# Kernel tuning notes

Hardware: AMD Instinct MI355X
Metric: run time of the kernel (lower is better)

## Reference

```python
import jax, jax.numpy as jnp
import numpy as np

N, E = 20000, 160000
F, H, OUT = 256, 8, 128
L = 6            # total layers -> 5 GAT layers
LM1 = L - 1
NGN = L // 3 + 1 # 3 GraphNorms
D = F // H       # 32 per head
GN_FREQ = 3
EPS = 1e-5


def setup_inputs() -> dict:
    key = jax.random.key(0)
    ks = jax.random.split(key, 12)
    x = jax.random.normal(ks[0], (N, 1), dtype=jnp.float32)
    edge_index = jax.random.randint(ks[1], (2, E), 0, N, dtype=jnp.int32)
    W0 = jax.random.normal(ks[2], (1, F), dtype=jnp.float32) * 0.1
    b0 = jnp.zeros((F,), jnp.float32)
    gat_lin = jax.random.normal(ks[3], (LM1, F, F), dtype=jnp.float32) * (1.0 / np.sqrt(F))
    att_src = jax.random.normal(ks[4], (LM1, H, D), dtype=jnp.float32) * 0.1
    att_dst = jax.random.normal(ks[5], (LM1, H, D), dtype=jnp.float32) * 0.1
    gat_bias = jnp.zeros((LM1, F), jnp.float32)
    gn_weight = jnp.ones((NGN, F), jnp.float32)
    gn_bias = jnp.zeros((NGN, F), jnp.float32)
    gn_mean_scale = jnp.ones((NGN, F), jnp.float32)
    lin_W = jax.random.normal(ks[6], (F, OUT), dtype=jnp.float32) * (1.0 / np.sqrt(F))
    lin_b = jnp.zeros((OUT,), jnp.float32)
    return {"x": x, "W0": W0, "b0": b0, "gat_lin": gat_lin, "att_src": att_src,
            "att_dst": att_dst, "gat_bias": gat_bias, "gn_weight": gn_weight,
            "gn_bias": gn_bias, "gn_mean_scale": gn_mean_scale,
            "lin_W": lin_W, "lin_b": lin_b, "edge_index": edge_index}


def _gcn_conv(x, W, b, src, dst, n):
    h = x @ W
    deg = jax.ops.segment_sum(jnp.ones(src.shape[0], h.dtype), dst, num_segments=n)
    dinv = jnp.where(deg > 0, jax.lax.rsqrt(deg), 0.0)
    norm = dinv[src] * dinv[dst]                      # [E']
    out = jax.ops.segment_sum(h[src] * norm[:, None], dst, num_segments=n)
    return out + b


def _gat_conv(x, W, a_src, a_dst, src, dst, n):
    # PyG GATConv (concat=True, negative_slope=0.2, self-loops in src/dst)
    h = (x @ W).reshape(n, H, D)
    s = jnp.einsum('nhd,hd->nh', h, a_src)            # [N,H]
    t = jnp.einsum('nhd,hd->nh', h, a_dst)
    e = jax.nn.leaky_relu(s[src] + t[dst], 0.2)       # [E',H]
    m = jax.ops.segment_max(e, dst, num_segments=n)   # per-dst softmax
    e = jnp.exp(e - m[dst])
    denom = jax.ops.segment_sum(e, dst, num_segments=n)
    alpha = e / (denom[dst] + 1e-16)
    out = jax.ops.segment_sum(h[src] * alpha[:, :, None], dst, num_segments=n)
    return out.reshape(n, F)


def _graph_norm(x, w, b, ms):
    # PyG GraphNorm with batch=None (single graph): per-feature stats over nodes
    mean = jnp.mean(x, axis=0)
    out = x - ms * mean
    var = jnp.mean(out * out, axis=0)
    return w * out * jax.lax.rsqrt(var + EPS) + b


def reference(x, W0, b0, gat_lin, att_src, att_dst, gat_bias, gn_weight, gn_bias,
              gn_mean_scale, lin_W, lin_b, edge_index):
    n = x.shape[0]
    loops = jnp.arange(n, dtype=edge_index.dtype)
    src = jnp.concatenate([edge_index[0], loops])
    dst = jnp.concatenate([edge_index[1], loops])
    h = jax.nn.relu(_gcn_conv(x, W0, b0, src, dst, n))
    for i in range(LM1):
        if i % GN_FREQ == 0:
            g = i // GN_FREQ
            h = _graph_norm(h, gn_weight[g], gn_bias[g], gn_mean_scale[g])
        out = _gat_conv(h, gat_lin[i], att_src[i], att_dst[i], src, dst, n)
        if i % GN_FREQ == 0:
            out = out + gat_bias[i]
        h = h + jax.nn.relu(out)
    return h @ lin_W + lin_b
```

## Files before the change

kernel.cpp:

```cpp
#include <hip/hip_runtime.h>
#include <hip/hip_bf16.h>
#include <stdint.h>

typedef float f32x4 __attribute__((ext_vector_type(4)));
typedef short s16x8 __attribute__((ext_vector_type(8)));

__device__ __forceinline__ float bf2f(unsigned short u) {
    union { unsigned int i; float f; } v; v.i = ((unsigned int)u) << 16; return v.f;
}
__device__ __forceinline__ unsigned short f2bf(float f) {
    union { float f; unsigned int i; } v; v.f = f;
    unsigned int x = v.i;
    return (unsigned short)((x + 0x7fffu + ((x >> 16) & 1u)) >> 16);
}
__device__ __forceinline__ void bfp(unsigned int u, float& lo, float& hi) {
    union { unsigned int i; float f; } a, b;
    a.i = u << 16; b.i = u & 0xffff0000u;
    lo = a.f; hi = b.f;
}
__device__ __forceinline__ void gload16(const void* g, void* l) {
    __builtin_amdgcn_global_load_lds(
        (const __attribute__((address_space(1))) void*)g,
        (__attribute__((address_space(3))) void*)l, 16, 0, 0);
}

__global__ void k_prep(const int* __restrict__ ei, int E, int* __restrict__ deg,
                       int CB,
                       const float* __restrict__ gat_lin,
                       const float* __restrict__ lin_W,
                       const float* __restrict__ att_src,
                       const float* __restrict__ att_dst,
                       unsigned short* __restrict__ Wt,
                       unsigned short* __restrict__ lt) {
    int bid = blockIdx.x;
    if (bid < CB) {
        int e = bid * 256 + threadIdx.x;
        if (e < E) atomicAdd(&deg[ei[E + e]], 1);
        return;
    }
    int idx = (bid - CB) * 256 + threadIdx.x;
    const int T1 = 5 * 65536;
    const int T2 = T1 + 128 * 256;
    const int T3 = T2 + 5 * 64 * 256;
    if (idx < T1) {
        int l = idx >> 16, r = idx & 0xFFFF;
        int k = r >> 8, nrow = r & 255;
        Wt[(size_t)l * 81920 + nrow * 256 + k] =
            f2bf(gat_lin[(size_t)l * 65536 + k * 256 + nrow]);
    } else if (idx < T2) {
        int j = idx - T1;
        int k = j >> 7, nrow = j & 127;
        lt[nrow * 256 + k] = f2bf(lin_W[(size_t)k * 128 + nrow]);
    } else if (idx < T3) {
        int j = idx - T2;
        int l = j >> 14, r = j & 16383;
        int row = r >> 8, k = r & 255;
        float v = 0.f;
        if (row < 16) {
            int head = row & 7;
            const float* a = (row < 8) ? (att_src + l * 256 + head * 32)
                                       : (att_dst + l * 256 + head * 32);
            const float* wr = gat_lin + (size_t)l * 65536 + k * 256 + head * 32;
#pragma unroll
            for (int d = 0; d < 32; ++d) v += wr[d] * a[d];
        }
        Wt[(size_t)l * 81920 + (256 + row) * 256 + k] = f2bf(v);
    }
}

__global__ __launch_bounds__(256) void k_emit(const int* __restrict__ deg,
                                              int* __restrict__ rowptr,
                                              int* __restrict__ wo,
                                              float* __restrict__ dinv, int n) {
    __shared__ int buf[256];
    int t = threadIdx.x;
    int bid = blockIdx.x;
    int lim = bid * 256;
    int s = 0;
    for (int i = t; i < lim; i += 256) s += deg[i] + 1;
    buf[t] = s;
    __syncthreads();
#pragma unroll
    for (int off = 128; off > 0; off >>= 1) {
        if (t < off) buf[t] += buf[t + off];
        __syncthreads();
    }
    int boff = buf[0];
    __syncthreads();
    int i = bid * 256 + t;
    int v = (i < n) ? deg[i] + 1 : 0;
    buf[t] = v;
    __syncthreads();
    for (int off = 1; off < 256; off <<= 1) {
        int add = (t >= off) ? buf[t - off] : 0;
        __syncthreads();
        buf[t] += add;
        __syncthreads();
    }
    if (i < n) {
        int excl = boff + buf[t] - v;
        rowptr[i] = excl;
        wo[i] = excl;
        dinv[i] = rsqrtf((float)v);
        if (i == n - 1) rowptr[n] = excl + v;
    }
}

__global__ void k_fill(const int* __restrict__ ei, int E, int n,
                       int* wo, int* srcs) {
    int e = blockIdx.x * blockDim.x + threadIdx.x;
    int EP = E + n;
    if (e >= EP) return;
    int s_, d_;
    if (e < E) { s_ = ei[e]; d_ = ei[E + e]; }
    else       { s_ = d_ = e - E; }
    int pos = atomicAdd(&wo[d_], 1);
    srcs[pos] = s_;
}

__global__ __launch_bounds__(256) void k_h0f(const float* __restrict__ x,
                                             const float* __restrict__ dinv,
                                             const int* __restrict__ rowptr,
                                             const int* __restrict__ srcs,
                                             const float* __restrict__ W0,
                                             const float* __restrict__ b0,
                                             unsigned short* __restrict__ hbf,
                                             int n, int Mpad) {
    int wave = threadIdx.x >> 6, lane = threadIdx.x & 63;
    int node = blockIdx.x * 4 + wave;
    if (node >= Mpad) return;
    size_t base = (size_t)node * 256 + lane * 4;
    if (node >= n) {
        ushort4 z = {0, 0, 0, 0};
        *reinterpret_cast<ushort4*>(hbf + base) = z;
        return;
    }
    int p0 = rowptr[node], p1 = rowptr[node + 1];
    float sum = 0.f;
    for (int p = p0 + lane; p < p1; p += 64) {
        int s = srcs[p];
        sum += x[s] * dinv[s];
    }
#pragma unroll
    for (int m = 1; m < 64; m <<= 1) sum += __shfl_xor(sum, m);
    float sv = sum * dinv[node];
    float4 wv = *reinterpret_cast<const float4*>(W0 + lane * 4);
    float4 bv = *reinterpret_cast<const float4*>(b0 + lane * 4);
    ushort4 o;
    o.x = f2bf(fmaxf(sv * wv.x + bv.x, 0.f));
    o.y = f2bf(fmaxf(sv * wv.y + bv.y, 0.f));
    o.z = f2bf(fmaxf(sv * wv.z + bv.z, 0.f));
    o.w = f2bf(fmaxf(sv * wv.w + bv.w, 0.f));
    *reinterpret_cast<ushort4*>(hbf + base) = o;
}

__global__ __launch_bounds__(256) void k_gn_reduce(const unsigned short* __restrict__ hbf,
                                                   float* sums, float* sumsq, int n) {
    int f = threadIdx.x;
    float s = 0.f, q = 0.f;
    for (int r = blockIdx.x; r < n; r += gridDim.x) {
        float v = bf2f(hbf[(size_t)r * 256 + f]);
        s += v; q += v * v;
    }
    atomicAdd(&sums[f], s);
    atomicAdd(&sumsq[f], q);
}

__global__ __launch_bounds__(256) void k_gnfold(const float* __restrict__ st,
                                                const float* __restrict__ w,
                                                const float* __restrict__ b,
                                                const float* __restrict__ ms,
                                                unsigned short* __restrict__ Wt,
                                                float* __restrict__ so,
                                                float* __restrict__ rowbias,
                                                float ninv) {
    __shared__ float red[256];
    int col = blockIdx.x, k = threadIdx.x;
    float mean = st[k] * ninv;
    float m2   = st[256 + k] * ninv;
    float msf  = ms[k];
    float var  = m2 + msf * mean * mean * (msf - 2.0f);
    float sc = w[k] * rsqrtf(var + 1e-5f);
    float of = b[k] - msf * mean * sc;
    size_t idx = (size_t)col * 256 + k;
    float wv = bf2f(Wt[idx]);
    red[k] = of * wv;
    __syncthreads();
#pragma unroll
    for (int off = 128; off > 0; off >>= 1) {
        if (k < off) red[k] += red[k + off];
        __syncthreads();
    }
    if (k == 0) rowbias[col] = red[0];
    Wt[idx] = f2bf(sc * wv);
    if (col == 0) { so[k] = sc; so[256 + k] = of; }
}

#define BM 64
__global__ __launch_bounds__(512) void k_gemm_mfma(
    const unsigned short* __restrict__ A,
    const unsigned short* __restrict__ Bt,
    unsigned short* __restrict__ Cb,
    float* __restrict__ Cf,
    float* __restrict__ sbuf,
    float* __restrict__ tbuf,
    const float* __restrict__ bias,
    const float* __restrict__ rowbias,
    int M, int ldc)
{
    __shared__ unsigned short As[64 * 256];
    __shared__ unsigned short Bs[64 * 256];
    const int tid = threadIdx.x;
    const int bm = blockIdx.x * BM;
    const int bn = blockIdx.y * 64;
    {
        const char* ga = (const char*)(A + (size_t)bm * 256);
        const char* gb = (const char*)(Bt + (size_t)bn * 256);
        char* la = (char*)As;
        char* lb = (char*)Bs;
#pragma unroll
        for (int i = 0; i < 4; ++i) {
            int o  = (i * 512 + tid) * 16;
            int so = o ^ (((o >> 9) & 7) << 4);
            gload16(ga + so, la + o);
            gload16(gb + so, lb + o);
        }
    }
    __syncthreads();

    const int lane = tid & 63;
    const int w  = tid >> 6;
    const int wm = (w >> 1) * 16;
    const int wn = (w & 1) * 32;
    const int r  = lane & 15, kb = lane >> 4;
    const int r4 = (lane >> 4) * 4, cc = lane & 15;
    const char* la = (const char*)As;
    const char* lb = (const char*)Bs;

    f32x4 acc[2] = {};
#pragma unroll
    for (int ks = 0; ks < 8; ++ks) {
        int row = wm + r;
        int c16 = (ks * 4 + kb) ^ (row & 7);
        s16x8 af = *(const s16x8*)(la + row * 512 + c16 * 16);
#pragma unroll
        for (int j = 0; j < 2; ++j) {
            int col = wn + j * 16 + r;
            int d16 = (ks * 4 + kb) ^ (col & 7);
            s16x8 bfr = *(const s16x8*)(lb + col * 512 + d16 * 16);
            acc[j] = __builtin_amdgcn_mfma_f32_16x16x32_bf16(af, bfr, acc[j], 0, 0, 0);
        }
    }
#pragma unroll
    for (int j = 0; j < 2; ++j) {
        int col = bn + wn + j * 16 + cc;
        float rb = rowbias ? rowbias[col] : 0.f;
#pragma unroll
        for (int q = 0; q < 4; ++q) {
            int row = bm + wm + r4 + q;
            float v = acc[j][q] + rb;
            if (Cb) {
                if (col < 256) {
                    Cb[(size_t)row * 256 + col] = f2bf(v);
                } else if (col < 264) {
                    sbuf[(size_t)row * 8 + (col - 256)] = v;
                } else if (col < 272) {
                    tbuf[(size_t)row * 8 + (col - 264)] = v;
                }
            } else if (row < M) {
                Cf[(size_t)row * ldc + col] = v + bias[col];
            }
        }
    }
}

__global__ __launch_bounds__(256) void k_fagg(const unsigned short* __restrict__ h1,
                                              const float* __restrict__ sbuf,
                                              const float* __restrict__ tbuf,
                                              const int* __restrict__ rowptr,
                                              const int* __restrict__ srcs,
                                              unsigned short* __restrict__ hbf,
                                              const float* __restrict__ bias,
                                              const float* __restrict__ so, int n) {
    int wave = threadIdx.x >> 6, lane = threadIdx.x & 63;
    int node = blockIdx.x * 4 + wave;
    if (node >= n) return;
    int p0 = rowptr[node], p1 = rowptr[node + 1];
    int hid = lane >> 5;
    int l5 = lane & 31;
    int fl = l5 * 8;
    int head = l5 >> 2;
    float tv = tbuf[node * 8 + head];
    float m = -1e30f, den = 0.f;
    float a0 = 0.f, a1 = 0.f, a2 = 0.f, a3 = 0.f;
    float a4 = 0.f, a5 = 0.f, a6 = 0.f, a7 = 0.f;
    int q = p0 + hid;
    for (; q + 6 < p1; q += 8) {
        int s0 = srcs[q], s1 = srcs[q + 2], s2 = srcs[q + 4], s3 = srcs[q + 6];
        float e0 = sbuf[s0 * 8 + head] + tv;
        float e1 = sbuf[s1 * 8 + head] + tv;
        float e2 = sbuf[s2 * 8 + head] + tv;
        float e3 = sbuf[s3 * 8 + head] + tv;
        uint4 v0 = *reinterpret_cast<const uint4*>(h1 + (size_t)s0 * 256 + fl);
        uint4 v1 = *reinterpret_cast<const uint4*>(h1 + (size_t)s1 * 256 + fl);
        uint4 v2 = *reinterpret_cast<const uint4*>(h1 + (size_t)s2 * 256 + fl);
        uint4 v3 = *reinterpret_cast<const uint4*>(h1 + (size_t)s3 * 256 + fl);
        e0 = (e0 > 0.f) ? e0 : 0.2f * e0;
        e1 = (e1 > 0.f) ? e1 : 0.2f * e1;
        e2 = (e2 > 0.f) ? e2 : 0.2f * e2;
        e3 = (e3 > 0.f) ? e3 : 0.2f * e3;
        float em = fmaxf(fmaxf(e0, e1), fmaxf(e2, e3));
        if (em > m + 8.f) {
            float sc = __expf(m - em);
            den *= sc;
            a0 *= sc; a1 *= sc; a2 *= sc; a3 *= sc;
            a4 *= sc; a5 *= sc; a6 *= sc; a7 *= sc;
            m = em;
        }
        float w0 = __expf(e0 - m), w1 = __expf(e1 - m);
        float w2 = __expf(e2 - m), w3 = __expf(e3 - m);
        den += (w0 + w1) + (w2 + w3);
        float fl0, fh0, fl1, fh1, fl2, fh2, fl3, fh3;
        bfp(v0.x, fl0, fh0); bfp(v1.x, fl1, fh1); bfp(v2.x, fl2, fh2); bfp(v3.x, fl3, fh3);
        a0 += (w0 * fl0 + w1 * fl1) + (w2 * fl2 + w3 * fl3);
        a1 += (w0 * fh0 + w1 * fh1) + (w2 * fh2 + w3 * fh3);
        bfp(v0.y, fl0, fh0); bfp(v1.y, fl1, fh1); bfp(v2.y, fl2, fh2); bfp(v3.y, fl3, fh3);
        a2 += (w0 * fl0 + w1 * fl1) + (w2 * fl2 + w3 * fl3);
        a3 += (w0 * fh0 + w1 * fh1) + (w2 * fh2 + w3 * fh3);
        bfp(v0.z, fl0, fh0); bfp(v1.z, fl1, fh1); bfp(v2.z, fl2, fh2); bfp(v3.z, fl3, fh3);
        a4 += (w0 * fl0 + w1 * fl1) + (w2 * fl2 + w3 * fl3);
        a5 += (w0 * fh0 + w1 * fh1) + (w2 * fh2 + w3 * fh3);
        bfp(v0.w, fl0, fh0); bfp(v1.w, fl1, fh1); bfp(v2.w, fl2, fh2); bfp(v3.w, fl3, fh3);
        a6 += (w0 * fl0 + w1 * fl1) + (w2 * fl2 + w3 * fl3);
        a7 += (w0 * fh0 + w1 * fh1) + (w2 * fh2 + w3 * fh3);
    }
    for (; q < p1; q += 2) {
        int s0 = srcs[q];
        float e0 = sbuf[s0 * 8 + head] + tv;
        uint4 v0 = *reinterpret_cast<const uint4*>(h1 + (size_t)s0 * 256 + fl);
        e0 = (e0 > 0.f) ? e0 : 0.2f * e0;
        if (e0 > m + 8.f) {
            float sc = __expf(m - e0);
            den *= sc;
            a0 *= sc; a1 *= sc; a2 *= sc; a3 *= sc;
            a4 *= sc; a5 *= sc; a6 *= sc; a7 *= sc;
            m = e0;
        }
        float w0 = __expf(e0 - m);
        den += w0;
        float f0l, f0h;
        bfp(v0.x, f0l, f0h); a0 += w0 * f0l; a1 += w0 * f0h;
        bfp(v0.y, f0l, f0h); a2 += w0 * f0l; a3 += w0 * f0h;
        bfp(v0.z, f0l, f0h); a4 += w0 * f0l; a5 += w0 * f0h;
        bfp(v0.w, f0l, f0h); a6 += w0 * f0l; a7 += w0 * f0h;
    }
    float mo = __shfl_xor(m, 32);
    float mm = fmaxf(m, mo);
    float sc = __expf(m - mm);
    den *= sc; den += __shfl_xor(den, 32);
    a0 *= sc; a0 += __shfl_xor(a0, 32);
    a1 *= sc; a1 += __shfl_xor(a1, 32);
    a2 *= sc; a2 += __shfl_xor(a2, 32);
    a3 *= sc; a3 += __shfl_xor(a3, 32);
    a4 *= sc; a4 += __shfl_xor(a4, 32);
    a5 *= sc; a5 += __shfl_xor(a5, 32);
    a6 *= sc; a6 += __shfl_xor(a6, 32);
    a7 *= sc; a7 += __shfl_xor(a7, 32);
    if (hid) return;
    float inv = 1.0f / (den + 1e-16f);
    a0 *= inv; a1 *= inv; a2 *= inv; a3 *= inv;
    a4 *= inv; a5 *= inv; a6 *= inv; a7 *= inv;
    float b_[8] = {0.f, 0.f, 0.f, 0.f, 0.f, 0.f, 0.f, 0.f};
    if (bias) {
        float4 blo = *reinterpret_cast<const float4*>(bias + fl);
        float4 bhi = *reinterpret_cast<const float4*>(bias + fl + 4);
        b_[0] = blo.x; b_[1] = blo.y; b_[2] = blo.z; b_[3] = blo.w;
        b_[4] = bhi.x; b_[5] = bhi.y; b_[6] = bhi.z; b_[7] = bhi.w;
    }
    size_t base = (size_t)node * 256 + fl;
    uint4 hv = *reinterpret_cast<const uint4*>(hbf + base);
    float h_[8];
    bfp(hv.x, h_[0], h_[1]); bfp(hv.y, h_[2], h_[3]);
    bfp(hv.z, h_[4], h_[5]); bfp(hv.w, h_[6], h_[7]);
    if (so) {
        float4 s0v = *reinterpret_cast<const float4*>(so + fl);
        float4 s1v = *reinterpret_cast<const float4*>(so + fl + 4);
        float4 o0v = *reinterpret_cast<const float4*>(so + 256 + fl);
        float4 o1v = *reinterpret_cast<const float4*>(so + 256 + fl + 4);
        h_[0] = h_[0] * s0v.x + o0v.x; h_[1] = h_[1] * s0v.y + o0v.y;
        h_[2] = h_[2] * s0v.z + o0v.z; h_[3] = h_[3] * s0v.w + o0v.w;
        h_[4] = h_[4] * s1v.x + o1v.x; h_[5] = h_[5] * s1v.y + o1v.y;
        h_[6] = h_[6] * s1v.z + o1v.z; h_[7] = h_[7] * s1v.w + o1v.w;
    }
    float r0 = h_[0] + fmaxf(a0 + b_[0], 0.f);
    float r1 = h_[1] + fmaxf(a1 + b_[1], 0.f);
    float r2 = h_[2] + fmaxf(a2 + b_[2], 0.f);
    float r3 = h_[3] + fmaxf(a3 + b_[3], 0.f);
    float r4 = h_[4] + fmaxf(a4 + b_[4], 0.f);
    float r5 = h_[5] + fmaxf(a5 + b_[5], 0.f);
    float r6 = h_[6] + fmaxf(a6 + b_[6], 0.f);
    float r7 = h_[7] + fmaxf(a7 + b_[7], 0.f);
    uint4 o;
    o.x = (unsigned int)f2bf(r0) | ((unsigned int)f2bf(r1) << 16);
    o.y = (unsigned int)f2bf(r2) | ((unsigned int)f2bf(r3) << 16);
    o.z = (unsigned int)f2bf(r4) | ((unsigned int)f2bf(r5) << 16);
    o.w = (unsigned int)f2bf(r6) | ((unsigned int)f2bf(r7) << 16);
    *reinterpret_cast<uint4*>(hbf + base) = o;
}

extern "C" void kernel_launch(void* const* d_in, const int* in_sizes, int n_in,
                              void* d_out, int out_size, void* d_ws, size_t ws_size,
                              hipStream_t stream) {
    const float* x        = (const float*)d_in[0];
    const float* W0       = (const float*)d_in[1];
    const float* b0       = (const float*)d_in[2];
    const float* gat_lin  = (const float*)d_in[3];
    const float* att_src  = (const float*)d_in[4];
    const float* att_dst  = (const float*)d_in[5];
    const float* gat_bias = (const float*)d_in[6];
    const float* gn_w     = (const float*)d_in[7];
    const float* gn_b     = (const float*)d_in[8];
    const float* gn_ms    = (const float*)d_in[9];
    const float* lin_W    = (const float*)d_in[10];
    const float* lin_b    = (const float*)d_in[11];
    const int*   ei       = (const int*)d_in[12];

    const int n  = in_sizes[0];
    const int E  = in_sizes[12] / 2;
    const int EP = E + n;
    const int Mpad = ((n + BM - 1) / BM) * BM;
    const int nb = (n + 255) / 256;

    char* w = (char*)d_ws;
    unsigned short* hbf = (unsigned short*)w; w += (size_t)Mpad * 256 * 2;
    unsigned short* h1  = (unsigned short*)w; w += (size_t)Mpad * 256 * 2;
    float* sbuf = (float*)w;                  w += (size_t)Mpad * 8 * 4;
    float* tbuf = (float*)w;                  w += (size_t)Mpad * 8 * 4;
    unsigned short* Wt = (unsigned short*)w;  w += (size_t)5 * 320 * 256 * 2;
    unsigned short* lt = (unsigned short*)w;  w += (size_t)128 * 256 * 2;
    float* scaleoff = (float*)w;              w += 1024 * 4;
    float* rowbias  = (float*)w;              w += 640 * 4;
    float* gnstat = (float*)w;                w += 1024 * 4;
    int* deg    = (int*)w;                    w += (size_t)n * 4;
    float* dinv = (float*)w;                  w += (size_t)n * 4;
    int* rowptr = (int*)w;                    w += ((size_t)(n + 1) * 4 + 15) / 16 * 16;
    int* wo     = (int*)w;                    w += (size_t)n * 4;
    int* srcs   = (int*)w;                    w += (size_t)EP * 4;

    const int B256 = 256;
    auto cdiv = [](int a, int b) { return (a + b - 1) / b; };

    hipMemsetAsync(gnstat, 0, 1024 * 4 + (size_t)n * 4, stream);

    const int CB = cdiv(E, B256);
    const int WPREP = 5 * 65536 + 128 * 256 + 5 * 64 * 256;
    k_prep<<<CB + cdiv(WPREP, B256), B256, 0, stream>>>(
        ei, E, deg, CB, gat_lin, lin_W, att_src, att_dst, Wt, lt);

    k_emit<<<nb, 256, 0, stream>>>(deg, rowptr, wo, dinv, n);
    k_fill<<<cdiv(EP, B256), B256, 0, stream>>>(ei, E, n, wo, srcs);

    k_h0f<<<cdiv(Mpad, 4), 256, 0, stream>>>(x, dinv, rowptr, srcs, W0, b0, hbf, n, Mpad);

    const float ninv = 1.0f / (float)n;
    const int gx = Mpad / BM;

    for (int i = 0; i < 5; ++i) {
        const float* rb = nullptr;
        const float* so = nullptr;
        if (i % 3 == 0) {
            int g = i / 3;
            k_gn_reduce<<<256, 256, 0, stream>>>(hbf, gnstat + g * 512,
                                                 gnstat + g * 512 + 256, n);
            k_gnfold<<<320, 256, 0, stream>>>(gnstat + g * 512, gn_w + g * 256,
                                              gn_b + g * 256, gn_ms + g * 256,
                                              Wt + (size_t)i * 81920,
                                              scaleoff + g * 512, rowbias + g * 320, ninv);
            rb = rowbias + g * 320;
            so = scaleoff + g * 512;
        }
        k_gemm_mfma<<<dim3(gx, 5), 512, 0, stream>>>(
            hbf, Wt + (size_t)i * 81920, h1, nullptr, sbuf, tbuf, nullptr, rb,
            n, 256);
        k_fagg<<<cdiv(n, 4), 256, 0, stream>>>(
            h1, sbuf, tbuf, rowptr, srcs, hbf,
            (i % 3 == 0) ? gat_bias + i * 256 : nullptr, so, n);
    }

    k_gemm_mfma<<<dim3(gx, 2), 512, 0, stream>>>(
        hbf, lt, nullptr, (float*)d_out, nullptr, nullptr, lin_b, nullptr,
        n, 128);
}
```

Measured before the change: 289.8 us.

## Fuse GAT aggregation with the following layer's projection GEMM

Adds a k_fused kernel in which each 512-thread block aggregates the attention-weighted neighbours for 64 nodes, applies the residual, bias and GraphNorm affine, and writes the bf16 result straight into LDS. It then loops over the weight panels to run the next layer's MFMA GEMM (or the final linear layer) from that LDS tile. This removes separate launches and the global round-trip of the aggregated features feeding the GEMM, and double-buffers h1, s and t across layers. The cost is far less parallelism for the latency-bound gather: the grid shrinks to one block per 64-row tile with 8 waves each processing 8 nodes sequentially, under a large LDS footprint per block.

```diff
diff --git a/kernel.cpp b/kernel.cpp
--- a/kernel.cpp
+++ b/kernel.cpp
@@ -196,95 +196,17 @@
     if (col == 0) { so[k] = sc; so[256 + k] = of; }
 }
 
-#define BM 64
-__global__ __launch_bounds__(512) void k_gemm_mfma(
-    const unsigned short* __restrict__ A,
-    const unsigned short* __restrict__ Bt,
-    unsigned short* __restrict__ Cb,
-    float* __restrict__ Cf,
-    float* __restrict__ sbuf,
-    float* __restrict__ tbuf,
+__device__ __forceinline__ uint4 fagg_node(
+    const unsigned short* __restrict__ h1,
+    const float* __restrict__ sbuf,
+    const float* __restrict__ tbuf,
+    const int* __restrict__ rowptr,
+    const int* __restrict__ srcs,
+    const unsigned short* __restrict__ hres,
     const float* __restrict__ bias,
-    const float* __restrict__ rowbias,
-    int M, int ldc)
+    const float* __restrict__ so,
+    int node, int lane)
 {
-    __shared__ unsigned short As[64 * 256];
-    __shared__ unsigned short Bs[64 * 256];
-    const int tid = threadIdx.x;
-    const int bm = blockIdx.x * BM;
-    const int bn = blockIdx.y * 64;
-    {
-        const char* ga = (const char*)(A + (size_t)bm * 256);
-        const char* gb = (const char*)(Bt + (size_t)bn * 256);
-        char* la = (char*)As;
-        char* lb = (char*)Bs;
-#pragma unroll
-        for (int i = 0; i < 4; ++i) {
-            int o  = (i * 512 + tid) * 16;
-            int so = o ^ (((o >> 9) & 7) << 4);
-            gload16(ga + so, la + o);
-            gload16(gb + so, lb + o);
-        }
-    }
-    __syncthreads();
-
-    const int lane = tid & 63;
-    const int w  = tid >> 6;
-    const int wm = (w >> 1) * 16;
-    const int wn = (w & 1) * 32;
-    const int r  = lane & 15, kb = lane >> 4;
-    const int r4 = (lane >> 4) * 4, cc = lane & 15;
-    const char* la = (const char*)As;
-    const char* lb = (const char*)Bs;
-
-    f32x4 acc[2] = {};
-#pragma unroll
-    for (int ks = 0; ks < 8; ++ks) {
-        int row = wm + r;
-        int c16 = (ks * 4 + kb) ^ (row & 7);
-        s16x8 af = *(const s16x8*)(la + row * 512 + c16 * 16);
-#pragma unroll
-        for (int j = 0; j < 2; ++j) {
-            int col = wn + j * 16 + r;
-            int d16 = (ks * 4 + kb) ^ (col & 7);
-            s16x8 bfr = *(const s16x8*)(lb + col * 512 + d16 * 16);
-            acc[j] = __builtin_amdgcn_mfma_f32_16x16x32_bf16(af, bfr, acc[j], 0, 0, 0);
-        }
-    }
-#pragma unroll
-    for (int j = 0; j < 2; ++j) {
-        int col = bn + wn + j * 16 + cc;
-        float rb = rowbias ? rowbias[col] : 0.f;
-#pragma unroll
-        for (int q = 0; q < 4; ++q) {
-            int row = bm + wm + r4 + q;
-            float v = acc[j][q] + rb;
-            if (Cb) {
-                if (col < 256) {
-                    Cb[(size_t)row * 256 + col] = f2bf(v);
-                } else if (col < 264) {
-                    sbuf[(size_t)row * 8 + (col - 256)] = v;
-                } else if (col < 272) {
-                    tbuf[(size_t)row * 8 + (col - 264)] = v;
-                }
-            } else if (row < M) {
-                Cf[(size_t)row * ldc + col] = v + bias[col];
-            }
-        }
-    }
-}
-
-__global__ __launch_bounds__(256) void k_fagg(const unsigned short* __restrict__ h1,
-                                              const float* __restrict__ sbuf,
-                                              const float* __restrict__ tbuf,
-                                              const int* __restrict__ rowptr,
-                                              const int* __restrict__ srcs,
-                                              unsigned short* __restrict__ hbf,
-                                              const float* __restrict__ bias,
-                                              const float* __restrict__ so, int n) {
-    int wave = threadIdx.x >> 6, lane = threadIdx.x & 63;
-    int node = blockIdx.x * 4 + wave;
-    if (node >= n) return;
     int p0 = rowptr[node], p1 = rowptr[node + 1];
     int hid = lane >> 5;
     int l5 = lane & 31;
@@ -366,46 +288,222 @@
     a5 *= sc; a5 += __shfl_xor(a5, 32);
     a6 *= sc; a6 += __shfl_xor(a6, 32);
     a7 *= sc; a7 += __shfl_xor(a7, 32);
-    if (hid) return;
-    float inv = 1.0f / (den + 1e-16f);
-    a0 *= inv; a1 *= inv; a2 *= inv; a3 *= inv;
-    a4 *= inv; a5 *= inv; a6 *= inv; a7 *= inv;
-    float b_[8] = {0.f, 0.f, 0.f, 0.f, 0.f, 0.f, 0.f, 0.f};
-    if (bias) {
-        float4 blo = *reinterpret_cast<const float4*>(bias + fl);
-        float4 bhi = *reinterpret_cast<const float4*>(bias + fl + 4);
-        b_[0] = blo.x; b_[1] = blo.y; b_[2] = blo.z; b_[3] = blo.w;
-        b_[4] = bhi.x; b_[5] = bhi.y; b_[6] = bhi.z; b_[7] = bhi.w;
-    }
-    size_t base = (size_t)node * 256 + fl;
-    uint4 hv = *reinterpret_cast<const uint4*>(hbf + base);
-    float h_[8];
-    bfp(hv.x, h_[0], h_[1]); bfp(hv.y, h_[2], h_[3]);
-    bfp(hv.z, h_[4], h_[5]); bfp(hv.w, h_[6], h_[7]);
-    if (so) {
-        float4 s0v = *reinterpret_cast<const float4*>(so + fl);
-        float4 s1v = *reinterpret_cast<const float4*>(so + fl + 4);
-        float4 o0v = *reinterpret_cast<const float4*>(so + 256 + fl);
-        float4 o1v = *reinterpret_cast<const float4*>(so + 256 + fl + 4);
-        h_[0] = h_[0] * s0v.x + o0v.x; h_[1] = h_[1] * s0v.y + o0v.y;
-        h_[2] = h_[2] * s0v.z + o0v.z; h_[3] = h_[3] * s0v.w + o0v.w;
-        h_[4] = h_[4] * s1v.x + o1v.x; h_[5] = h_[5] * s1v.y + o1v.y;
-        h_[6] = h_[6] * s1v.z + o1v.z; h_[7] = h_[7] * s1v.w + o1v.w;
-    }
-    float r0 = h_[0] + fmaxf(a0 + b_[0], 0.f);
-    float r1 = h_[1] + fmaxf(a1 + b_[1], 0.f);
-    float r2 = h_[2] + fmaxf(a2 + b_[2], 0.f);
-    float r3 = h_[3] + fmaxf(a3 + b_[3], 0.f);
-    float r4 = h_[4] + fmaxf(a4 + b_[4], 0.f);
-    float r5 = h_[5] + fmaxf(a5 + b_[5], 0.f);
-    float r6 = h_[6] + fmaxf(a6 + b_[6], 0.f);
-    float r7 = h_[7] + fmaxf(a7 + b_[7], 0.f);
-    uint4 o;
-    o.x = (unsigned int)f2bf(r0) | ((unsigned int)f2bf(r1) << 16);
-    o.y = (unsigned int)f2bf(r2) | ((unsigned int)f2bf(r3) << 16);
-    o.z = (unsigned int)f2bf(r4) | ((unsigned int)f2bf(r5) << 16);
-    o.w = (unsigned int)f2bf(r6) | ((unsigned int)f2bf(r7) << 16);
-    *reinterpret_cast<uint4*>(hbf + base) = o;
+    uint4 o = {0, 0, 0, 0};
+    if (!hid) {
+        float inv = 1.0f / (den + 1e-16f);
+        a0 *= inv; a1 *= inv; a2 *= inv; a3 *= inv;
+        a4 *= inv; a5 *= inv; a6 *= inv; a7 *= inv;
+        float b_[8] = {0.f, 0.f, 0.f, 0.f, 0.f, 0.f, 0.f, 0.f};
+        if (bias) {
+            float4 blo = *reinterpret_cast<const float4*>(bias + fl);
+            float4 bhi = *reinterpret_cast<const float4*>(bias + fl + 4);
+            b_[0] = blo.x; b_[1] = blo.y; b_[2] = blo.z; b_[3] = blo.w;
+            b_[4] = bhi.x; b_[5] = bhi.y; b_[6] = bhi.z; b_[7] = bhi.w;
+        }
+        size_t base = (size_t)node * 256 + fl;
+        uint4 hv = *reinterpret_cast<const uint4*>(hres + base);
+        float h_[8];
+        bfp(hv.x, h_[0], h_[1]); bfp(hv.y, h_[2], h_[3]);
+        bfp(hv.z, h_[4], h_[5]); bfp(hv.w, h_[6], h_[7]);
+        if (so) {
+            float4 s0v = *reinterpret_cast<const float4*>(so + fl);
+            float4 s1v = *reinterpret_cast<const float4*>(so + fl + 4);
+            float4 o0v = *reinterpret_cast<const float4*>(so + 256 + fl);
+            float4 o1v = *reinterpret_cast<const float4*>(so + 256 + fl + 4);
+            h_[0] = h_[0] * s0v.x + o0v.x; h_[1] = h_[1] * s0v.y + o0v.y;
+            h_[2] = h_[2] * s0v.z + o0v.z; h_[3] = h_[3] * s0v.w + o0v.w;
+            h_[4] = h_[4] * s1v.x + o1v.x; h_[5] = h_[5] * s1v.y + o1v.y;
+            h_[6] = h_[6] * s1v.z + o1v.z; h_[7] = h_[7] * s1v.w + o1v.w;
+        }
+        float r0 = h_[0] + fmaxf(a0 + b_[0], 0.f);
+        float r1 = h_[1] + fmaxf(a1 + b_[1], 0.f);
+        float r2 = h_[2] + fmaxf(a2 + b_[2], 0.f);
+        float r3 = h_[3] + fmaxf(a3 + b_[3], 0.f);
+        float r4 = h_[4] + fmaxf(a4 + b_[4], 0.f);
+        float r5 = h_[5] + fmaxf(a5 + b_[5], 0.f);
+        float r6 = h_[6] + fmaxf(a6 + b_[6], 0.f);
+        float r7 = h_[7] + fmaxf(a7 + b_[7], 0.f);
+        o.x = (unsigned int)f2bf(r0) | ((unsigned int)f2bf(r1) << 16);
+        o.y = (unsigned int)f2bf(r2) | ((unsigned int)f2bf(r3) << 16);
+        o.z = (unsigned int)f2bf(r4) | ((unsigned int)f2bf(r5) << 16);
+        o.w = (unsigned int)f2bf(r6) | ((unsigned int)f2bf(r7) << 16);
+    }
+    return o;
+}
+
+__global__ __launch_bounds__(256) void k_fagg(const unsigned short* __restrict__ h1,
+                                              const float* __restrict__ sbuf,
+                                              const float* __restrict__ tbuf,
+                                              const int* __restrict__ rowptr,
+                                              const int* __restrict__ srcs,
+                                              unsigned short* __restrict__ hbf,
+                                              const float* __restrict__ bias,
+                                              const float* __restrict__ so, int n) {
+    int wave = threadIdx.x >> 6, lane = threadIdx.x & 63;
+    int node = blockIdx.x * 4 + wave;
+    if (node >= n) return;
+    uint4 o = fagg_node(h1, sbuf, tbuf, rowptr, srcs, hbf, bias, so, node, lane);
+    if (!(lane >> 5))
+        *reinterpret_cast<uint4*>(hbf + (size_t)node * 256 + (lane & 31) * 8) = o;
+}
+
+#define BM 64
+__global__ __launch_bounds__(512) void k_gemm_mfma(
+    const unsigned short* __restrict__ A,
+    const unsigned short* __restrict__ Bt,
+    unsigned short* __restrict__ Cb,
+    float* __restrict__ sbuf,
+    float* __restrict__ tbuf,
+    const float* __restrict__ rowbias)
+{
+    __shared__ unsigned short As[64 * 256];
+    __shared__ unsigned short Bs[64 * 256];
+    const int tid = threadIdx.x;
+    const int bm = blockIdx.x * BM;
+    const int bn = blockIdx.y * 64;
+    {
+        const char* ga = (const char*)(A + (size_t)bm * 256);
+        const char* gb = (const char*)(Bt + (size_t)bn * 256);
+#pragma unroll
+        for (int i = 0; i < 4; ++i) {
+            int o  = (i * 512 + tid) * 16;
+            int so = o ^ (((o >> 9) & 7) << 4);
+            gload16(ga + so, (char*)As + o);
+            gload16(gb + so, (char*)Bs + o);
+        }
+    }
+    __syncthreads();
+
+    const int lane = tid & 63;
+    const int w  = tid >> 6;
+    const int wm = (w >> 1) * 16;
+    const int wn = (w & 1) * 32;
+    const int r  = lane & 15, kb = lane >> 4;
+    const int r4 = (lane >> 4) * 4, cc = lane & 15;
+
+    f32x4 acc[2] = {};
+#pragma unroll
+    for (int ks = 0; ks < 8; ++ks) {
+        int row = wm + r;
+        int c16 = (ks * 4 + kb) ^ (row & 7);
+        s16x8 af = *(const s16x8*)((char*)As + row * 512 + c16 * 16);
+#pragma unroll
+        for (int j = 0; j < 2; ++j) {
+            int col = wn + j * 16 + r;
+            int d16 = (ks * 4 + kb) ^ (col & 7);
+            s16x8 bfr = *(const s16x8*)((char*)Bs + col * 512 + d16 * 16);
+            acc[j] = __builtin_amdgcn_mfma_f32_16x16x32_bf16(af, bfr, acc[j], 0, 0, 0);
+        }
+    }
+#pragma unroll
+    for (int j = 0; j < 2; ++j) {
+        int col = bn + wn + j * 16 + cc;
+        float rb = rowbias ? rowbias[col] : 0.f;
+#pragma unroll
+        for (int q = 0; q < 4; ++q) {
+            int row = bm + wm + r4 + q;
+            float v = acc[j][q] + rb;
+            if (col < 256) {
+                Cb[(size_t)row * 256 + col] = f2bf(v);
+            } else if (col < 264) {
+                sbuf[(size_t)row * 8 + (col - 256)] = v;
+            } else if (col < 272) {
+                tbuf[(size_t)row * 8 + (col - 264)] = v;
+            }
+        }
+    }
+}
+
+__global__ __launch_bounds__(512) void k_fused(
+    const unsigned short* __restrict__ h1in,
+    const float* __restrict__ sbin,
+    const float* __restrict__ tbin,
+    const int* __restrict__ rowptr,
+    const int* __restrict__ srcs,
+    const unsigned short* __restrict__ hres,
+    unsigned short* __restrict__ hout,
+    const float* __restrict__ bias,
+    const float* __restrict__ so,
+    const unsigned short* __restrict__ Bt,
+    unsigned short* __restrict__ Cb,
+    float* __restrict__ Cf,
+    float* __restrict__ sbout, float* __restrict__ tbout,
+    const float* __restrict__ lbias,
+    int n, int npan, int ldc)
+{
+    __shared__ unsigned short As[64 * 256];
+    __shared__ unsigned short Bs[64 * 256];
+    const int tid = threadIdx.x;
+    const int wid = tid >> 6, lane = tid & 63;
+    const int bm = blockIdx.x * 64;
+    const int l5 = lane & 31, hid = lane >> 5;
+
+    for (int j = 0; j < 8; ++j) {
+        int node = bm + wid * 8 + j;
+        int lrow = wid * 8 + j;
+        uint4 o4 = {0, 0, 0, 0};
+        if (node < n)
+            o4 = fagg_node(h1in, sbin, tbin, rowptr, srcs, hres, bias, so, node, lane);
+        if (!hid) {
+            int c = l5 ^ (lrow & 7);
+            *reinterpret_cast<uint4*>((char*)As + lrow * 512 + c * 16) = o4;
+            if (hout && node < n)
+                *reinterpret_cast<uint4*>(hout + (size_t)node * 256 + l5 * 8) = o4;
+        }
+    }
+    __syncthreads();
+
+    const int wm = (wid >> 1) * 16;
+    const int wn = (wid & 1) * 32;
+    const int r  = lane & 15, kb = lane >> 4;
+    const int r4 = (lane >> 4) * 4, cc = lane & 15;
+    for (int pan = 0; pan < npan; ++pan) {
+        if (pan) __syncthreads();
+        {
+            const char* gb = (const char*)(Bt + (size_t)pan * 16384);
+#pragma unroll
+            for (int i = 0; i < 4; ++i) {
+                int o  = (i * 512 + tid) * 16;
+                int sw = o ^ (((o >> 9) & 7) << 4);
+                gload16(gb + sw, (char*)Bs + o);
+            }
+        }
+        __syncthreads();
+        f32x4 acc[2] = {};
+#pragma unroll
+        for (int ks = 0; ks < 8; ++ks) {
+            int row = wm + r;
+            int c16 = (ks * 4 + kb) ^ (row & 7);
+            s16x8 af = *(const s16x8*)((char*)As + row * 512 + c16 * 16);
+#pragma unroll
+            for (int jj = 0; jj < 2; ++jj) {
+                int col = wn + jj * 16 + r;
+                int d16 = (ks * 4 + kb) ^ (col & 7);
+                s16x8 bfr = *(const s16x8*)((char*)Bs + col * 512 + d16 * 16);
+                acc[jj] = __builtin_amdgcn_mfma_f32_16x16x32_bf16(af, bfr, acc[jj], 0, 0, 0);
+            }
+        }
+#pragma unroll
+        for (int jj = 0; jj < 2; ++jj) {
+            int col = pan * 64 + wn + jj * 16 + cc;
+#pragma unroll
+            for (int q = 0; q < 4; ++q) {
+                int row = bm + wm + r4 + q;
+                float v = acc[jj][q];
+                if (Cb) {
+                    if (col < 256) {
+                        Cb[(size_t)row * 256 + col] = f2bf(v);
+                    } else if (col < 264) {
+                        sbout[(size_t)row * 8 + (col - 256)] = v;
+                    } else if (col < 272) {
+                        tbout[(size_t)row * 8 + (col - 264)] = v;
+                    }
+                } else if (row < n) {
+                    Cf[(size_t)row * ldc + col] = v + lbias[col];
+                }
+            }
+        }
+    }
 }
 
 extern "C" void kernel_launch(void* const* d_in, const int* in_sizes, int n_in,
@@ -432,20 +530,23 @@
     const int nb = (n + 255) / 256;
 
     char* w = (char*)d_ws;
-    unsigned short* hbf = (unsigned short*)w; w += (size_t)Mpad * 256 * 2;
-    unsigned short* h1  = (unsigned short*)w; w += (size_t)Mpad * 256 * 2;
-    float* sbuf = (float*)w;                  w += (size_t)Mpad * 8 * 4;
-    float* tbuf = (float*)w;                  w += (size_t)Mpad * 8 * 4;
-    unsigned short* Wt = (unsigned short*)w;  w += (size_t)5 * 320 * 256 * 2;
-    unsigned short* lt = (unsigned short*)w;  w += (size_t)128 * 256 * 2;
-    float* scaleoff = (float*)w;              w += 1024 * 4;
-    float* rowbias  = (float*)w;              w += 640 * 4;
-    float* gnstat = (float*)w;                w += 1024 * 4;
-    int* deg    = (int*)w;                    w += (size_t)n * 4;
-    float* dinv = (float*)w;                  w += (size_t)n * 4;
-    int* rowptr = (int*)w;                    w += ((size_t)(n + 1) * 4 + 15) / 16 * 16;
-    int* wo     = (int*)w;                    w += (size_t)n * 4;
-    int* srcs   = (int*)w;                    w += (size_t)EP * 4;
+    unsigned short* hbf = (unsigned short*)w;  w += (size_t)Mpad * 256 * 2;
+    unsigned short* h1a = (unsigned short*)w;  w += (size_t)Mpad * 256 * 2;
+    unsigned short* h1b = (unsigned short*)w;  w += (size_t)Mpad * 256 * 2;
+    float* sba = (float*)w;                    w += (size_t)Mpad * 8 * 4;
+    float* sbb = (float*)w;                    w += (size_t)Mpad * 8 * 4;
+    float* tba = (float*)w;                    w += (size_t)Mpad * 8 * 4;
+    float* tbb = (float*)w;                    w += (size_t)Mpad * 8 * 4;
+    unsigned short* Wt = (unsigned short*)w;   w += (size_t)5 * 320 * 256 * 2;
+    unsigned short* lt = (unsigned short*)w;   w += (size_t)128 * 256 * 2;
+    float* scaleoff = (float*)w;               w += 1024 * 4;
+    float* rowbias  = (float*)w;               w += 640 * 4;
+    float* gnstat = (float*)w;                 w += 1024 * 4;
+    int* deg    = (int*)w;                     w += (size_t)n * 4;
+    float* dinv = (float*)w;                   w += (size_t)n * 4;
+    int* rowptr = (int*)w;                     w += ((size_t)(n + 1) * 4 + 15) / 16 * 16;
+    int* wo     = (int*)w;                     w += (size_t)n * 4;
+    int* srcs   = (int*)w;                     w += (size_t)EP * 4;
 
     const int B256 = 256;
     auto cdiv = [](int a, int b) { return (a + b - 1) / b; };
@@ -459,35 +560,38 @@
 
     k_emit<<<nb, 256, 0, stream>>>(deg, rowptr, wo, dinv, n);
     k_fill<<<cdiv(EP, B256), B256, 0, stream>>>(ei, E, n, wo, srcs);
-
     k_h0f<<<cdiv(Mpad, 4), 256, 0, stream>>>(x, dinv, rowptr, srcs, W0, b0, hbf, n, Mpad);
 
     const float ninv = 1.0f / (float)n;
     const int gx = Mpad / BM;
 
-    for (int i = 0; i < 5; ++i) {
-        const float* rb = nullptr;
-        const float* so = nullptr;
-        if (i % 3 == 0) {
-            int g = i / 3;
-            k_gn_reduce<<<256, 256, 0, stream>>>(hbf, gnstat + g * 512,
-                                                 gnstat + g * 512 + 256, n);
-            k_gnfold<<<320, 256, 0, stream>>>(gnstat + g * 512, gn_w + g * 256,
-                                              gn_b + g * 256, gn_ms + g * 256,
-                                              Wt + (size_t)i * 81920,
-                                              scaleoff + g * 512, rowbias + g * 320, ninv);
-            rb = rowbias + g * 320;
-            so = scaleoff + g * 512;
-        }
-        k_gemm_mfma<<<dim3(gx, 5), 512, 0, stream>>>(
-            hbf, Wt + (size_t)i * 81920, h1, nullptr, sbuf, tbuf, nullptr, rb,
-            n, 256);
-        k_fagg<<<cdiv(n, 4), 256, 0, stream>>>(
-            h1, sbuf, tbuf, rowptr, srcs, hbf,
-            (i % 3 == 0) ? gat_bias + i * 256 : nullptr, so, n);
-    }
-
-    k_gemm_mfma<<<dim3(gx, 2), 512, 0, stream>>>(
-        hbf, lt, nullptr, (float*)d_out, nullptr, nullptr, lin_b, nullptr,
-        n, 128);
-}
+    k_gn_reduce<<<256, 256, 0, stream>>>(hbf, gnstat, gnstat + 256, n);
+    k_gnfold<<<320, 256, 0, stream>>>(gnstat, gn_w, gn_b, gn_ms,
+                                      Wt, scaleoff, rowbias, ninv);
+    k_gemm_mfma<<<dim3(gx, 5), 512, 0, stream>>>(hbf, Wt, h1a, sba, tba, rowbias);
+
+    k_fused<<<gx, 512, 0, stream>>>(h1a, sba, tba, rowptr, srcs, hbf, hbf,
+                                    gat_bias, scaleoff,
+                                    Wt + (size_t)1 * 81920, h1b, nullptr, sbb, tbb,
+                                    nullptr, n, 5, 256);
+    k_fused<<<gx, 512, 0, stream>>>(h1b, sbb, tbb, rowptr, srcs, hbf, hbf,
+                                    nullptr, nullptr,
+                                    Wt + (size_t)2 * 81920, h1a, nullptr, sba, tba,
+                                    nullptr, n, 5, 256);
+    k_fagg<<<cdiv(n, 4), 256, 0, stream>>>(h1a, sba, tba, rowptr, srcs, hbf,
+                                           nullptr, nullptr, n);
+    k_gn_reduce<<<256, 256, 0, stream>>>(hbf, gnstat + 512, gnstat + 768, n);
+    k_gnfold<<<320, 256, 0, stream>>>(gnstat + 512, gn_w + 256, gn_b + 256,
+                                      gn_ms + 256, Wt + (size_t)3 * 81920,
+                                      scaleoff + 512, rowbias + 320, ninv);
+    k_gemm_mfma<<<dim3(gx, 5), 512, 0, stream>>>(hbf, Wt + (size_t)3 * 81920,
+                                                 h1b, sbb, tbb, rowbias + 320);
+    k_fused<<<gx, 512, 0, stream>>>(h1b, sbb, tbb, rowptr, srcs, hbf, hbf,
+                                    gat_bias + 3 * 256, scaleoff + 512,
+                                    Wt + (size_t)4 * 81920, h1a, nullptr, sba, tba,
+                                    nullptr, n, 5, 256);
+    k_fused<<<gx, 512, 0, stream>>>(h1a, sba, tba, rowptr, srcs, hbf, nullptr,
+                                    nullptr, nullptr,
+                                    lt, nullptr, (float*)d_out, nullptr, nullptr,
+                                    lin_b, n, 2, 128);
+}
```

Result: slower. 326.2 us (+12.6%).
